# Performance work log

Hardware: AMD Instinct MI355X
Metric: run time of the kernel (lower is better)

The kernel has to match this reference:

```python
import jax, jax.numpy as jnp
import numpy as np
from jax import lax

DIM = 256
HEADS = 8
SR = 4
EPS = 1e-5
SCALE = (DIM // HEADS) ** -0.5


def _dwconv(x, wgt, stride, pad):
    # x: (B,C,H,W), wgt: (C,1,kh,kw) depthwise
    return lax.conv_general_dilated(
        x, wgt, (stride, stride), [(pad, pad), (pad, pad)],
        feature_group_count=x.shape[1],
        dimension_numbers=("NCHW", "OIHW", "NCHW"))


def _bn(x, g, b, m, v):
    # eval-mode batchnorm folded to per-channel scale/shift
    s = g / jnp.sqrt(v + EPS)
    return x * s[:, None, None] + (b - m * s)[:, None, None]


def setup_inputs() -> dict:
    key = jax.random.key(0)
    ks = jax.random.split(key, 16)
    b, h, w = 8, 64, 64
    c = DIM
    n = h * w

    def rn(k, shape, s=0.05):
        return jax.random.normal(k, shape, jnp.float32) * s

    return dict(
        x=jax.random.normal(ks[0], (b, n, c), jnp.float32),
        h=h, w=w,
        Wq=rn(ks[1], (c, c)), bq=rn(ks[2], (c,)),
        Wkv=rn(ks[3], (2 * c, c)), bkv=rn(ks[4], (2 * c,)),
        sr_w1=rn(ks[5], (c, 1, SR + 3, SR + 3), 0.1),
        bn1_gamma=1.0 + rn(ks[6], (c,)), bn1_beta=rn(ks[7], (c,)),
        bn1_mean=rn(ks[8], (c,)), bn1_var=jnp.abs(1.0 + rn(ks[9], (c,))),
        sr_w2=1.0 + rn(ks[10], (c,), 0.2),  # 1x1 depthwise conv == per-channel scale
        bn2_gamma=1.0 + rn(ks[11], (c,)), bn2_beta=rn(ks[12], (c,)),
        bn2_mean=rn(ks[13], (c,)), bn2_var=jnp.abs(1.0 + rn(ks[14], (c,))),
        local_w=rn(ks[15], (c, 1, 3, 3), 0.1),
        local_b=jnp.zeros((c,), jnp.float32),
    )


def reference(x, h, w, Wq, bq, Wkv, bkv, sr_w1, bn1_gamma, bn1_beta, bn1_mean,
              bn1_var, sr_w2, bn2_gamma, bn2_beta, bn2_mean, bn2_var,
              local_w, local_b):
    b, n, c = x.shape
    hd = c // HEADS
    xi = x.transpose(0, 2, 1).reshape(b, c, h, w)  # (b,c,h,w)

    # q projection (1x1 conv == channel matmul)
    q = jnp.einsum("bchw,dc->bdhw", xi, Wq) + bq[None, :, None, None]
    q = q.reshape(b, HEADS, hd, n).transpose(0, 1, 3, 2)  # (b,H,n,hd)

    # spatial reduction: dwconv7 s4 + BN + GELU + dw1x1 + BN
    kv = _dwconv(xi, sr_w1, SR, (SR + 3) // 2)
    kv = _bn(kv, bn1_gamma, bn1_beta, bn1_mean, bn1_var)
    kv = jax.nn.gelu(kv, approximate=False)
    kv = kv * sr_w2[None, :, None, None]
    kv = _bn(kv, bn2_gamma, bn2_beta, bn2_mean, bn2_var)

    # residual local depthwise 3x3 conv
    kv = _dwconv(kv, local_w, 1, 1) + local_b[None, :, None, None] + kv

    # kv projection and split
    kvp = jnp.einsum("bchw,dc->bdhw", kv, Wkv) + bkv[None, :, None, None]
    k_, v_ = jnp.split(kvp, 2, axis=1)
    m = k_.shape[2] * k_.shape[3]
    k_ = k_.reshape(b, HEADS, hd, m)                       # (b,H,hd,m)
    v_ = v_.reshape(b, HEADS, hd, m).transpose(0, 1, 3, 2)  # (b,H,m,hd)

    attn = jax.nn.softmax(jnp.einsum("bhnd,bhdm->bhnm", q, k_) * SCALE, axis=-1)
    out = jnp.einsum("bhnm,bhmd->bhnd", attn, v_)           # (b,H,n,hd)
    out = out.transpose(0, 1, 3, 2).reshape(b, c, n).transpose(0, 2, 1)
    return out
```

## Files before the change

### kernel.cpp

```cpp
#include <hip/hip_runtime.h>
#include <math.h>

typedef __bf16 bf16;
typedef bf16 bf16x4 __attribute__((ext_vector_type(4)));
typedef bf16 bf16x8 __attribute__((ext_vector_type(8)));
typedef float f32x4 __attribute__((ext_vector_type(4)));

static_assert(sizeof(bf16x8) == 16, "bf16x8 must be 16B");

#define QSCALE (0.17677669529663687f * 1.4426950408889634f)

__device__ __forceinline__ f32x4 mfma16(bf16x8 a, bf16x8 b, f32x4 c) {
  return __builtin_amdgcn_mfma_f32_16x16x32_bf16(a, b, c, 0, 0, 0);
}

__global__ __launch_bounds__(256) void k_cvt(
    const float* __restrict__ Wq, const float* __restrict__ Wkv,
    const float* __restrict__ w7, bf16* __restrict__ Wqb,
    bf16* __restrict__ Wkvb, float* __restrict__ w7t) {
  const int tid = threadIdx.x;
  const int blk = blockIdx.x;
  if (blk < 96) {
    const float* src;
    bf16* dst;
    if (blk < 32) {
      const int idx = blk * 256 + tid;
      src = Wq + (size_t)idx * 8;
      dst = Wqb + (size_t)idx * 8;
    } else {
      const int idx = (blk - 32) * 256 + tid;
      src = Wkv + (size_t)idx * 8;
      dst = Wkvb + (size_t)idx * 8;
    }
    const float4 a = ((const float4*)src)[0];
    const float4 b = ((const float4*)src)[1];
    bf16x8 r;
    r[0] = (bf16)a.x; r[1] = (bf16)a.y; r[2] = (bf16)a.z; r[3] = (bf16)a.w;
    r[4] = (bf16)b.x; r[5] = (bf16)b.y; r[6] = (bf16)b.z; r[7] = (bf16)b.w;
    *(bf16x8*)dst = r;
  } else {
    const int c = tid;
    #pragma unroll
    for (int tap = 0; tap < 49; tap++)
      w7t[tap * 256 + c] = w7[c * 49 + tap];
  }
}

__global__ __launch_bounds__(256) void k_sr(
    const float* __restrict__ x, const float* __restrict__ w7t,
    const float* __restrict__ g1, const float* __restrict__ b1,
    const float* __restrict__ m1, const float* __restrict__ v1,
    const float* __restrict__ sw2,
    const float* __restrict__ g2, const float* __restrict__ b2,
    const float* __restrict__ m2, const float* __restrict__ v2,
    bf16* __restrict__ kv1) {
  __shared__ float part[4][256];
  const int tid = threadIdx.x;
  const int team = tid >> 6, g = tid & 63;
  const int c0 = g * 4;
  const int blk = blockIdx.x;
  const int b = blk & 7, m = blk >> 3;
  const int oy = m >> 4, ox = m & 15;

  float4 xv[13], wv[13];
  float msk[13];
  #pragma unroll
  for (int j = 0; j < 13; j++) {
    const int tap = team + j * 4;
    const int ky = tap / 7, kx = tap - ky * 7;
    const int iy = oy * 4 - 3 + ky, ix = ox * 4 - 3 + kx;
    msk[j] = (tap < 49 && iy >= 0 && iy < 64 && ix >= 0 && ix < 64) ? 1.f : 0.f;
    const int iyc = iy < 0 ? 0 : (iy > 63 ? 63 : iy);
    const int ixc = ix < 0 ? 0 : (ix > 63 ? 63 : ix);
    const int tc = tap > 48 ? 48 : tap;
    xv[j] = *(const float4*)(x + ((size_t)b * 4096 + iyc * 64 + ixc) * 256 + c0);
    wv[j] = *(const float4*)(w7t + tc * 256 + c0);
  }
  float a0 = 0.f, a1 = 0.f, a2 = 0.f, a3 = 0.f;
  #pragma unroll
  for (int j = 0; j < 13; j++) {
    a0 += xv[j].x * wv[j].x * msk[j];
    a1 += xv[j].y * wv[j].y * msk[j];
    a2 += xv[j].z * wv[j].z * msk[j];
    a3 += xv[j].w * wv[j].w * msk[j];
  }
  *(f32x4*)&part[team][c0] = (f32x4){a0, a1, a2, a3};
  __syncthreads();
  const int c = tid;
  float y = part[0][c] + part[1][c] + part[2][c] + part[3][c];
  float s = g1[c] / sqrtf(v1[c] + 1e-5f);
  y = y * s + (b1[c] - m1[c] * s);
  y = 0.5f * y * (1.f + erff(y * 0.70710678118654752f));
  y *= sw2[c];
  s = g2[c] / sqrtf(v2[c] + 1e-5f);
  y = y * s + (b2[c] - m2[c] * s);
  kv1[((size_t)b * 256 + m) * 256 + c] = (bf16)y;
}

__global__ __launch_bounds__(256) void k_localkv(
    const bf16* __restrict__ kv1, const float* __restrict__ w3,
    const float* __restrict__ lb, const bf16* __restrict__ Wkvb,
    const float* __restrict__ bkv, bf16* __restrict__ k_a,
    bf16* __restrict__ v_b) {
  __shared__ bf16 halo[3][10][256];
  __shared__ float rows[8][256];
  const int c = threadIdx.x;
  const int mt = blockIdx.x;
  const int b = blockIdx.y;
  const int oy = mt >> 1, o0 = (mt & 1) * 8;

  #pragma unroll
  for (int p = 0; p < 30; p++) {
    const int dy = p / 10, xi = p - dy * 10;
    const int iy = oy - 1 + dy, ix = o0 - 1 + xi;
    const bool ok = (iy >= 0 && iy < 16 && ix >= 0 && ix < 16);
    const int iyc = ok ? iy : 0, ixc = ok ? ix : 0;
    const bf16 v = kv1[((size_t)b * 256 + iyc * 16 + ixc) * 256 + c];
    halo[dy][xi][c] = ok ? v : (bf16)0.f;
  }
  float w3f[9];
  #pragma unroll
  for (int t = 0; t < 9; t++) w3f[t] = w3[c * 9 + t];
  const float lbf = lb[c];
  __syncthreads();

  #pragma unroll
  for (int r = 0; r < 8; r++) {
    float acc = lbf + (float)halo[1][r + 1][c];
    #pragma unroll
    for (int ky = 0; ky < 3; ky++)
      #pragma unroll
      for (int kx = 0; kx < 3; kx++)
        acc += (float)halo[ky][r + kx][c] * w3f[ky * 3 + kx];
    rows[r][c] = acc;
  }
  __syncthreads();

  const int tid = c;
  float acck[8] = {0}, accv[8] = {0};
  for (int oc = 0; oc < 32; oc++) {
    const bf16x8 w0 = *(const bf16x8*)(Wkvb + (size_t)tid * 256 + oc * 8);
    const bf16x8 w1 = *(const bf16x8*)(Wkvb + ((size_t)tid + 256) * 256 + oc * 8);
    float wf0[8], wf1[8];
    #pragma unroll
    for (int j = 0; j < 8; j++) { wf0[j] = (float)w0[j]; wf1[j] = (float)w1[j]; }
    #pragma unroll
    for (int r = 0; r < 8; r++) {
      const float4* rp = (const float4*)&rows[r][oc * 8];
      const float4 ra = rp[0], rb = rp[1];
      const float rv[8] = {ra.x, ra.y, ra.z, ra.w, rb.x, rb.y, rb.z, rb.w};
      #pragma unroll
      for (int j = 0; j < 8; j++) {
        acck[r] += wf0[j] * rv[j];
        accv[r] += wf1[j] * rv[j];
      }
    }
  }
  const float bk = bkv[tid], bv = bkv[tid + 256];
  const int h = tid >> 5, d = tid & 31;
  #pragma unroll
  for (int r = 0; r < 8; r++) {
    const int m = (oy * 16 + o0) + r;
    k_a[(((size_t)b * 8 + h) * 256 + m) * 32 + d] = (bf16)(acck[r] + bk);
    v_b[(((size_t)b * 8 + h) * 32 + d) * 256 + m] = (bf16)(accv[r] + bv);
  }
}

__global__ __launch_bounds__(256) void k_qproj(
    const float* __restrict__ x, const bf16* __restrict__ Wqb,
    const float* __restrict__ bq, bf16* __restrict__ q_ws) {
  __shared__ bf16 xs[32 * 264];
  const int tid = threadIdx.x, wv = tid >> 6, lane = tid & 63;
  const int qd = lane >> 4, l15 = lane & 15;
  const size_t rowbase = (size_t)blockIdx.x * 32;

  #pragma unroll
  for (int it = 0; it < 4; it++) {
    const int idx = it * 256 + tid;
    const int lr = idx >> 5, pos = idx & 31;
    const float* src = x + (rowbase + lr) * 256 + pos * 8;
    const float4 a = ((const float4*)src)[0];
    const float4 b = ((const float4*)src)[1];
    bf16x8 r;
    r[0] = (bf16)a.x; r[1] = (bf16)a.y; r[2] = (bf16)a.z; r[3] = (bf16)a.w;
    r[4] = (bf16)b.x; r[5] = (bf16)b.y; r[6] = (bf16)b.z; r[7] = (bf16)b.w;
    *(bf16x8*)(xs + lr * 264 + pos * 8) = r;
  }
  __syncthreads();

  f32x4 acc0[4], acc1[4];
  #pragma unroll
  for (int dt = 0; dt < 4; dt++) {
    acc0[dt] = (f32x4){0.f, 0.f, 0.f, 0.f};
    acc1[dt] = (f32x4){0.f, 0.f, 0.f, 0.f};
  }
  #pragma unroll 2
  for (int kc = 0; kc < 8; kc++) {
    const bf16x8 a0 = *(const bf16x8*)(xs + l15 * 264 + kc * 32 + qd * 8);
    const bf16x8 a1 = *(const bf16x8*)(xs + (16 + l15) * 264 + kc * 32 + qd * 8);
    #pragma unroll
    for (int dt = 0; dt < 4; dt++) {
      const int d = wv * 64 + dt * 16 + l15;
      const bf16x8 bb = *(const bf16x8*)(Wqb + (size_t)d * 256 + kc * 32 + qd * 8);
      acc0[dt] = mfma16(a0, bb, acc0[dt]);
      acc1[dt] = mfma16(a1, bb, acc1[dt]);
    }
  }
  #pragma unroll
  for (int dt = 0; dt < 4; dt++) {
    const int d = wv * 64 + dt * 16 + l15;
    const float bias = bq[d];
    const int h = d >> 5, dl = d & 31;
    #pragma unroll
    for (int r = 0; r < 4; r++) {
      const size_t row0 = rowbase + qd * 4 + r;
      const size_t row1 = rowbase + 16 + qd * 4 + r;
      q_ws[(((row0 >> 12) * 8 + h) * 4096 + (row0 & 4095)) * 32 + dl] =
          (bf16)((acc0[dt][r] + bias) * QSCALE);
      q_ws[(((row1 >> 12) * 8 + h) * 4096 + (row1 & 4095)) * 32 + dl] =
          (bf16)((acc1[dt][r] + bias) * QSCALE);
    }
  }
}

__global__ __launch_bounds__(256) void k_attn(
    const bf16* __restrict__ q_ws, const bf16* __restrict__ k_a,
    const bf16* __restrict__ v_b, float* __restrict__ out) {
  const int tid = threadIdx.x;
  const int wv = tid >> 6, lane = tid & 63;
  const int qd = lane >> 4, l15 = lane & 15;
  const int b = blockIdx.z, h = blockIdx.y;
  const int bh = b * 8 + h;
  const int n_base = blockIdx.x * 256 + wv * 64;

  const bf16* qb = q_ws + ((size_t)bh * 4096 + n_base) * 32;
  bf16x8 qf[4];
  #pragma unroll
  for (int qi = 0; qi < 4; qi++)
    qf[qi] = *(const bf16x8*)(qb + (size_t)(qi * 16 + l15) * 32 + qd * 8);

  const bf16* kb = k_a + (size_t)bh * 256 * 32;
  const bf16* vb = v_b + (size_t)bh * 32 * 256;

  f32x4 acc[4][2];
  float lr[4] = {0.f, 0.f, 0.f, 0.f};
  #pragma unroll
  for (int qi = 0; qi < 4; qi++) {
    acc[qi][0] = (f32x4){0.f, 0.f, 0.f, 0.f};
    acc[qi][1] = (f32x4){0.f, 0.f, 0.f, 0.f};
  }
  const int kperm = 8 * (l15 >> 2) + (l15 & 3);

  bf16x8 ka0 = *(const bf16x8*)(kb + (size_t)kperm * 32 + qd * 8);
  bf16x8 ka1 = *(const bf16x8*)(kb + (size_t)(kperm + 4) * 32 + qd * 8);
  bf16x8 va0 = *(const bf16x8*)(vb + (size_t)l15 * 256 + qd * 8);
  bf16x8 va1 = *(const bf16x8*)(vb + (size_t)(16 + l15) * 256 + qd * 8);

  for (int ch = 0; ch < 8; ch++) {
    const int cn = (ch < 7 ? ch + 1 : 7) * 32;
    const bf16x8 nk0 = *(const bf16x8*)(kb + (size_t)(cn + kperm) * 32 + qd * 8);
    const bf16x8 nk1 = *(const bf16x8*)(kb + (size_t)(cn + kperm + 4) * 32 + qd * 8);
    const bf16x8 nv0 = *(const bf16x8*)(vb + (size_t)l15 * 256 + cn + qd * 8);
    const bf16x8 nv1 = *(const bf16x8*)(vb + (size_t)(16 + l15) * 256 + cn + qd * 8);
    const f32x4 z = (f32x4){0.f, 0.f, 0.f, 0.f};
    #pragma unroll
    for (int qi = 0; qi < 4; qi++) {
      f32x4 s0 = mfma16(ka0, qf[qi], z);
      f32x4 s1 = mfma16(ka1, qf[qi], z);
      float p[8], ls = 0.f;
      #pragma unroll
      for (int j = 0; j < 4; j++) {
        p[j] = __builtin_amdgcn_exp2f(fminf(s0[j], 80.f));
        p[4 + j] = __builtin_amdgcn_exp2f(fminf(s1[j], 80.f));
      }
      #pragma unroll
      for (int j = 0; j < 8; j++) ls += p[j];
      lr[qi] += ls;
      bf16x8 pb;
      #pragma unroll
      for (int j = 0; j < 8; j++) pb[j] = (bf16)p[j];
      acc[qi][0] = mfma16(va0, pb, acc[qi][0]);
      acc[qi][1] = mfma16(va1, pb, acc[qi][1]);
    }
    ka0 = nk0; ka1 = nk1; va0 = nv0; va1 = nv1;
  }
  #pragma unroll
  for (int qi = 0; qi < 4; qi++) {
    float l = lr[qi];
    l += __shfl_xor(l, 16, 64);
    l += __shfl_xor(l, 32, 64);
    const float inv = 1.f / l;
    const int nn = n_base + qi * 16 + l15;
    float* ob = out + (size_t)(b * 4096 + nn) * 256 + h * 32;
    #pragma unroll
    for (int t = 0; t < 2; t++) {
      *(float4*)(ob + t * 16 + qd * 4) =
          (float4){acc[qi][t][0] * inv, acc[qi][t][1] * inv,
                   acc[qi][t][2] * inv, acc[qi][t][3] * inv};
    }
  }
}

extern "C" void kernel_launch(void* const* d_in, const int* in_sizes, int n_in,
                              void* d_out, int out_size, void* d_ws, size_t ws_size,
                              hipStream_t stream) {
  const float* x      = (const float*)d_in[0];
  const float* Wq     = (const float*)d_in[3];
  const float* bq     = (const float*)d_in[4];
  const float* Wkv    = (const float*)d_in[5];
  const float* bkv    = (const float*)d_in[6];
  const float* sr_w1  = (const float*)d_in[7];
  const float* bn1_g  = (const float*)d_in[8];
  const float* bn1_b  = (const float*)d_in[9];
  const float* bn1_m  = (const float*)d_in[10];
  const float* bn1_v  = (const float*)d_in[11];
  const float* sw2    = (const float*)d_in[12];
  const float* bn2_g  = (const float*)d_in[13];
  const float* bn2_b  = (const float*)d_in[14];
  const float* bn2_m  = (const float*)d_in[15];
  const float* bn2_v  = (const float*)d_in[16];
  const float* lw     = (const float*)d_in[17];
  const float* lb     = (const float*)d_in[18];

  const int B = in_sizes[0] / (4096 * 256);

  bf16* Wqb  = (bf16*)d_ws;
  bf16* Wkvb = Wqb + 65536;
  float* w7t = (float*)(Wkvb + 131072);
  bf16* kv1  = (bf16*)(w7t + 12544);
  bf16* k_a  = kv1 + (size_t)B * 256 * 256;
  bf16* v_b  = k_a + (size_t)B * 8 * 256 * 32;
  bf16* q_ws = v_b + (size_t)B * 8 * 32 * 256;

  k_cvt<<<dim3(97), 256, 0, stream>>>(Wq, Wkv, sr_w1, Wqb, Wkvb, w7t);
  k_sr<<<dim3(256 * B), 256, 0, stream>>>(x, w7t, bn1_g, bn1_b, bn1_m, bn1_v,
                                          sw2, bn2_g, bn2_b, bn2_m, bn2_v, kv1);
  k_localkv<<<dim3(32, B), 256, 0, stream>>>(kv1, lw, lb, Wkvb, bkv, k_a, v_b);
  k_qproj<<<dim3(B * 128), 256, 0, stream>>>(x, Wqb, bq, q_ws);
  k_attn<<<dim3(16, 8, B), 256, 0, stream>>>(q_ws, k_a, v_b, (float*)d_out);
}
```

Baseline: 186.7 us.

## Fuse q projection into attention and merge weight conversion with spatial reduction

The q projection is now computed inside the attention kernel for each (batch, head, 256-row tile). x is staged through shared memory as bf16, and the scaled q values are placed in LDS instead of a global workspace. This removes the q workspace write and read and one launch, but each x tile is now re-read once per head. The weight-conversion kernel is merged with the spatial-reduction kernel, and the 7x7 weight transpose pass is dropped in favour of strided reads of the original weights. This saves another launch and a small workspace.

```diff
diff --git a/kernel.cpp b/kernel.cpp
--- a/kernel.cpp
+++ b/kernel.cpp
@@ -14,21 +14,30 @@
   return __builtin_amdgcn_mfma_f32_16x16x32_bf16(a, b, c, 0, 0, 0);
 }
 
-__global__ __launch_bounds__(256) void k_cvt(
+__global__ __launch_bounds__(256) void k_pre(
+    const float* __restrict__ x, const float* __restrict__ w7,
+    const float* __restrict__ g1, const float* __restrict__ b1,
+    const float* __restrict__ m1, const float* __restrict__ v1,
+    const float* __restrict__ sw2,
+    const float* __restrict__ g2, const float* __restrict__ b2,
+    const float* __restrict__ m2, const float* __restrict__ v2,
     const float* __restrict__ Wq, const float* __restrict__ Wkv,
-    const float* __restrict__ w7, bf16* __restrict__ Wqb,
-    bf16* __restrict__ Wkvb, float* __restrict__ w7t) {
+    bf16* __restrict__ Wqb, bf16* __restrict__ Wkvb,
+    bf16* __restrict__ kv1, int nsr) {
+  __shared__ float part[4][256];
   const int tid = threadIdx.x;
   const int blk = blockIdx.x;
-  if (blk < 96) {
+
+  if (blk >= nsr) {
+    const int wb = blk - nsr;
     const float* src;
     bf16* dst;
-    if (blk < 32) {
-      const int idx = blk * 256 + tid;
+    if (wb < 32) {
+      const int idx = wb * 256 + tid;
       src = Wq + (size_t)idx * 8;
       dst = Wqb + (size_t)idx * 8;
     } else {
-      const int idx = (blk - 32) * 256 + tid;
+      const int idx = (wb - 32) * 256 + tid;
       src = Wkv + (size_t)idx * 8;
       dst = Wkvb + (size_t)idx * 8;
     }
@@ -38,32 +47,15 @@
     r[0] = (bf16)a.x; r[1] = (bf16)a.y; r[2] = (bf16)a.z; r[3] = (bf16)a.w;
     r[4] = (bf16)b.x; r[5] = (bf16)b.y; r[6] = (bf16)b.z; r[7] = (bf16)b.w;
     *(bf16x8*)dst = r;
-  } else {
-    const int c = tid;
-    #pragma unroll
-    for (int tap = 0; tap < 49; tap++)
-      w7t[tap * 256 + c] = w7[c * 49 + tap];
-  }
-}
-
-__global__ __launch_bounds__(256) void k_sr(
-    const float* __restrict__ x, const float* __restrict__ w7t,
-    const float* __restrict__ g1, const float* __restrict__ b1,
-    const float* __restrict__ m1, const float* __restrict__ v1,
-    const float* __restrict__ sw2,
-    const float* __restrict__ g2, const float* __restrict__ b2,
-    const float* __restrict__ m2, const float* __restrict__ v2,
-    bf16* __restrict__ kv1) {
-  __shared__ float part[4][256];
-  const int tid = threadIdx.x;
+    return;
+  }
   const int team = tid >> 6, g = tid & 63;
   const int c0 = g * 4;
-  const int blk = blockIdx.x;
   const int b = blk & 7, m = blk >> 3;
   const int oy = m >> 4, ox = m & 15;
 
-  float4 xv[13], wv[13];
-  float msk[13];
+  float4 xv[13];
+  float wj[13][4], msk[13];
   #pragma unroll
   for (int j = 0; j < 13; j++) {
     const int tap = team + j * 4;
@@ -74,15 +66,16 @@
     const int ixc = ix < 0 ? 0 : (ix > 63 ? 63 : ix);
     const int tc = tap > 48 ? 48 : tap;
     xv[j] = *(const float4*)(x + ((size_t)b * 4096 + iyc * 64 + ixc) * 256 + c0);
-    wv[j] = *(const float4*)(w7t + tc * 256 + c0);
+    #pragma unroll
+    for (int i = 0; i < 4; i++) wj[j][i] = w7[(c0 + i) * 49 + tc];
   }
   float a0 = 0.f, a1 = 0.f, a2 = 0.f, a3 = 0.f;
   #pragma unroll
   for (int j = 0; j < 13; j++) {
-    a0 += xv[j].x * wv[j].x * msk[j];
-    a1 += xv[j].y * wv[j].y * msk[j];
-    a2 += xv[j].z * wv[j].z * msk[j];
-    a3 += xv[j].w * wv[j].w * msk[j];
+    a0 += xv[j].x * wj[j][0] * msk[j];
+    a1 += xv[j].y * wj[j][1] * msk[j];
+    a2 += xv[j].z * wj[j][2] * msk[j];
+    a3 += xv[j].w * wj[j][3] * msk[j];
   }
   *(f32x4*)&part[team][c0] = (f32x4){a0, a1, a2, a3};
   __syncthreads();
@@ -166,78 +159,66 @@
   }
 }
 
-__global__ __launch_bounds__(256) void k_qproj(
+__global__ __launch_bounds__(256) void k_qattn(
     const float* __restrict__ x, const bf16* __restrict__ Wqb,
-    const float* __restrict__ bq, bf16* __restrict__ q_ws) {
-  __shared__ bf16 xs[32 * 264];
-  const int tid = threadIdx.x, wv = tid >> 6, lane = tid & 63;
-  const int qd = lane >> 4, l15 = lane & 15;
-  const size_t rowbase = (size_t)blockIdx.x * 32;
-
-  #pragma unroll
-  for (int it = 0; it < 4; it++) {
-    const int idx = it * 256 + tid;
-    const int lr = idx >> 5, pos = idx & 31;
-    const float* src = x + (rowbase + lr) * 256 + pos * 8;
-    const float4 a = ((const float4*)src)[0];
-    const float4 b = ((const float4*)src)[1];
-    bf16x8 r;
-    r[0] = (bf16)a.x; r[1] = (bf16)a.y; r[2] = (bf16)a.z; r[3] = (bf16)a.w;
-    r[4] = (bf16)b.x; r[5] = (bf16)b.y; r[6] = (bf16)b.z; r[7] = (bf16)b.w;
-    *(bf16x8*)(xs + lr * 264 + pos * 8) = r;
-  }
-  __syncthreads();
-
-  f32x4 acc0[4], acc1[4];
-  #pragma unroll
-  for (int dt = 0; dt < 4; dt++) {
-    acc0[dt] = (f32x4){0.f, 0.f, 0.f, 0.f};
-    acc1[dt] = (f32x4){0.f, 0.f, 0.f, 0.f};
-  }
-  #pragma unroll 2
-  for (int kc = 0; kc < 8; kc++) {
-    const bf16x8 a0 = *(const bf16x8*)(xs + l15 * 264 + kc * 32 + qd * 8);
-    const bf16x8 a1 = *(const bf16x8*)(xs + (16 + l15) * 264 + kc * 32 + qd * 8);
-    #pragma unroll
-    for (int dt = 0; dt < 4; dt++) {
-      const int d = wv * 64 + dt * 16 + l15;
-      const bf16x8 bb = *(const bf16x8*)(Wqb + (size_t)d * 256 + kc * 32 + qd * 8);
-      acc0[dt] = mfma16(a0, bb, acc0[dt]);
-      acc1[dt] = mfma16(a1, bb, acc1[dt]);
-    }
-  }
-  #pragma unroll
-  for (int dt = 0; dt < 4; dt++) {
-    const int d = wv * 64 + dt * 16 + l15;
-    const float bias = bq[d];
-    const int h = d >> 5, dl = d & 31;
-    #pragma unroll
-    for (int r = 0; r < 4; r++) {
-      const size_t row0 = rowbase + qd * 4 + r;
-      const size_t row1 = rowbase + 16 + qd * 4 + r;
-      q_ws[(((row0 >> 12) * 8 + h) * 4096 + (row0 & 4095)) * 32 + dl] =
-          (bf16)((acc0[dt][r] + bias) * QSCALE);
-      q_ws[(((row1 >> 12) * 8 + h) * 4096 + (row1 & 4095)) * 32 + dl] =
-          (bf16)((acc1[dt][r] + bias) * QSCALE);
-    }
-  }
-}
-
-__global__ __launch_bounds__(256) void k_attn(
-    const bf16* __restrict__ q_ws, const bf16* __restrict__ k_a,
+    const float* __restrict__ bq, const bf16* __restrict__ k_a,
     const bf16* __restrict__ v_b, float* __restrict__ out) {
+  __shared__ bf16 xs[256 * 40];
   const int tid = threadIdx.x;
   const int wv = tid >> 6, lane = tid & 63;
   const int qd = lane >> 4, l15 = lane & 15;
-  const int b = blockIdx.z, h = blockIdx.y;
+  const int nt = blockIdx.x, h = blockIdx.y, b = blockIdx.z;
   const int bh = b * 8 + h;
-  const int n_base = blockIdx.x * 256 + wv * 64;
-
-  const bf16* qb = q_ws + ((size_t)bh * 4096 + n_base) * 32;
+  const size_t brow0 = (size_t)b * 4096 + nt * 256;
+
+  f32x4 dq0[4], dq1[4];
+  #pragma unroll
+  for (int qi = 0; qi < 4; qi++) {
+    dq0[qi] = (f32x4){0.f, 0.f, 0.f, 0.f};
+    dq1[qi] = (f32x4){0.f, 0.f, 0.f, 0.f};
+  }
+  for (int kc = 0; kc < 8; kc++) {
+    __syncthreads();
+    #pragma unroll
+    for (int j = 0; j < 8; j++) {
+      const int e = j * 1024 + tid * 4;
+      const int r = e >> 5, c = e & 31;
+      const float4 v = *(const float4*)(x + (brow0 + r) * 256 + kc * 32 + c);
+      bf16x4 bv;
+      bv[0] = (bf16)v.x; bv[1] = (bf16)v.y; bv[2] = (bf16)v.z; bv[3] = (bf16)v.w;
+      *(bf16x4*)(xs + r * 40 + c) = bv;
+    }
+    __syncthreads();
+    const bf16x8 a0 = *(const bf16x8*)(Wqb + (size_t)(h * 32 + l15) * 256 + kc * 32 + qd * 8);
+    const bf16x8 a1 = *(const bf16x8*)(Wqb + (size_t)(h * 32 + 16 + l15) * 256 + kc * 32 + qd * 8);
+    #pragma unroll
+    for (int qi = 0; qi < 4; qi++) {
+      const bf16x8 bb = *(const bf16x8*)(xs + (wv * 64 + qi * 16 + l15) * 40 + qd * 8);
+      dq0[qi] = mfma16(a0, bb, dq0[qi]);
+      dq1[qi] = mfma16(a1, bb, dq1[qi]);
+    }
+  }
+  const float4 bq0 = *(const float4*)(bq + h * 32 + qd * 4);
+  const float4 bq1 = *(const float4*)(bq + h * 32 + 16 + qd * 4);
+  bf16* ql = xs + (size_t)wv * 64 * 40;
+  #pragma unroll
+  for (int qi = 0; qi < 4; qi++) {
+    bf16x4 q0, q1;
+    q0[0] = (bf16)((dq0[qi][0] + bq0.x) * QSCALE);
+    q0[1] = (bf16)((dq0[qi][1] + bq0.y) * QSCALE);
+    q0[2] = (bf16)((dq0[qi][2] + bq0.z) * QSCALE);
+    q0[3] = (bf16)((dq0[qi][3] + bq0.w) * QSCALE);
+    q1[0] = (bf16)((dq1[qi][0] + bq1.x) * QSCALE);
+    q1[1] = (bf16)((dq1[qi][1] + bq1.y) * QSCALE);
+    q1[2] = (bf16)((dq1[qi][2] + bq1.z) * QSCALE);
+    q1[3] = (bf16)((dq1[qi][3] + bq1.w) * QSCALE);
+    *(bf16x4*)(ql + (qi * 16 + l15) * 40 + qd * 4) = q0;
+    *(bf16x4*)(ql + (qi * 16 + l15) * 40 + 16 + qd * 4) = q1;
+  }
   bf16x8 qf[4];
   #pragma unroll
   for (int qi = 0; qi < 4; qi++)
-    qf[qi] = *(const bf16x8*)(qb + (size_t)(qi * 16 + l15) * 32 + qd * 8);
+    qf[qi] = *(const bf16x8*)(ql + (qi * 16 + l15) * 40 + qd * 8);
 
   const bf16* kb = k_a + (size_t)bh * 256 * 32;
   const bf16* vb = v_b + (size_t)bh * 32 * 256;
@@ -290,7 +271,7 @@
     l += __shfl_xor(l, 16, 64);
     l += __shfl_xor(l, 32, 64);
     const float inv = 1.f / l;
-    const int nn = n_base + qi * 16 + l15;
+    const int nn = nt * 256 + wv * 64 + qi * 16 + l15;
     float* ob = out + (size_t)(b * 4096 + nn) * 256 + h * 32;
     #pragma unroll
     for (int t = 0; t < 2; t++) {
@@ -326,16 +307,16 @@
 
   bf16* Wqb  = (bf16*)d_ws;
   bf16* Wkvb = Wqb + 65536;
-  float* w7t = (float*)(Wkvb + 131072);
-  bf16* kv1  = (bf16*)(w7t + 12544);
+  bf16* kv1  = Wkvb + 131072;
   bf16* k_a  = kv1 + (size_t)B * 256 * 256;
   bf16* v_b  = k_a + (size_t)B * 8 * 256 * 32;
-  bf16* q_ws = v_b + (size_t)B * 8 * 32 * 256;
-
-  k_cvt<<<dim3(97), 256, 0, stream>>>(Wq, Wkv, sr_w1, Wqb, Wkvb, w7t);
-  k_sr<<<dim3(256 * B), 256, 0, stream>>>(x, w7t, bn1_g, bn1_b, bn1_m, bn1_v,
-                                          sw2, bn2_g, bn2_b, bn2_m, bn2_v, kv1);
+
+  const int nsr = 256 * B;
+
+  k_pre<<<dim3(nsr + 96), 256, 0, stream>>>(
+      x, sr_w1, bn1_g, bn1_b, bn1_m, bn1_v, sw2, bn2_g, bn2_b, bn2_m, bn2_v,
+      Wq, Wkv, Wqb, Wkvb, kv1, nsr);
   k_localkv<<<dim3(32, B), 256, 0, stream>>>(kv1, lw, lb, Wkvb, bkv, k_a, v_b);
-  k_qproj<<<dim3(B * 128), 256, 0, stream>>>(x, Wqb, bq, q_ws);
-  k_attn<<<dim3(16, 8, B), 256, 0, stream>>>(q_ws, k_a, v_b, (float*)d_out);
-}
+  k_qattn<<<dim3(16, 8, B), 256, 0, stream>>>(x, Wqb, bq, k_a, v_b,
+                                              (float*)d_out);
+}
```

New measurement: 232.0 us. 1.24x slower.

## Merge weight conversion with SR conv and fuse localkv with qproj launch

Applied to the files above, without the earlier changes.

The weight-convert kernel and the spatial-reduction conv kernel are combined into one launch, and the local-conv/kv-projection and q-projection kernels share a second launch selected by block index. The 7x7 weight transpose pass is dropped: each team now handles a contiguous run of taps and reads the weights straight from the original layout. Going from five launches to three is meant to cut launch overhead and tail gaps and to let the independent q projection overlap the small kv work. In exchange, the per-thread weight reads are strided and uncoalesced, and the combined kernels have to reserve the larger shared-memory footprint.

```diff
diff --git a/kernel.cpp b/kernel.cpp
--- a/kernel.cpp
+++ b/kernel.cpp
@@ -14,21 +14,30 @@
   return __builtin_amdgcn_mfma_f32_16x16x32_bf16(a, b, c, 0, 0, 0);
 }
 
-__global__ __launch_bounds__(256) void k_cvt(
+__global__ __launch_bounds__(256) void k_pre(
+    const float* __restrict__ x, const float* __restrict__ w7,
+    const float* __restrict__ g1, const float* __restrict__ b1,
+    const float* __restrict__ m1, const float* __restrict__ v1,
+    const float* __restrict__ sw2,
+    const float* __restrict__ g2, const float* __restrict__ b2,
+    const float* __restrict__ m2, const float* __restrict__ v2,
     const float* __restrict__ Wq, const float* __restrict__ Wkv,
-    const float* __restrict__ w7, bf16* __restrict__ Wqb,
-    bf16* __restrict__ Wkvb, float* __restrict__ w7t) {
+    bf16* __restrict__ Wqb, bf16* __restrict__ Wkvb,
+    bf16* __restrict__ kv1, int nsr) {
+  __shared__ float part[4][256];
   const int tid = threadIdx.x;
   const int blk = blockIdx.x;
-  if (blk < 96) {
+
+  if (blk >= nsr) {
+    const int wb = blk - nsr;
     const float* src;
     bf16* dst;
-    if (blk < 32) {
-      const int idx = blk * 256 + tid;
+    if (wb < 32) {
+      const int idx = wb * 256 + tid;
       src = Wq + (size_t)idx * 8;
       dst = Wqb + (size_t)idx * 8;
     } else {
-      const int idx = (blk - 32) * 256 + tid;
+      const int idx = (wb - 32) * 256 + tid;
       src = Wkv + (size_t)idx * 8;
       dst = Wkvb + (size_t)idx * 8;
     }
@@ -38,51 +47,42 @@
     r[0] = (bf16)a.x; r[1] = (bf16)a.y; r[2] = (bf16)a.z; r[3] = (bf16)a.w;
     r[4] = (bf16)b.x; r[5] = (bf16)b.y; r[6] = (bf16)b.z; r[7] = (bf16)b.w;
     *(bf16x8*)dst = r;
-  } else {
-    const int c = tid;
-    #pragma unroll
-    for (int tap = 0; tap < 49; tap++)
-      w7t[tap * 256 + c] = w7[c * 49 + tap];
-  }
-}
-
-__global__ __launch_bounds__(256) void k_sr(
-    const float* __restrict__ x, const float* __restrict__ w7t,
-    const float* __restrict__ g1, const float* __restrict__ b1,
-    const float* __restrict__ m1, const float* __restrict__ v1,
-    const float* __restrict__ sw2,
-    const float* __restrict__ g2, const float* __restrict__ b2,
-    const float* __restrict__ m2, const float* __restrict__ v2,
-    bf16* __restrict__ kv1) {
-  __shared__ float part[4][256];
-  const int tid = threadIdx.x;
+    return;
+  }
   const int team = tid >> 6, g = tid & 63;
   const int c0 = g * 4;
-  const int blk = blockIdx.x;
+  const int base = (team == 0) ? 0 : (1 + team * 12);
+  const int cnt  = (team == 0) ? 13 : 12;
   const int b = blk & 7, m = blk >> 3;
   const int oy = m >> 4, ox = m & 15;
 
-  float4 xv[13], wv[13];
+  float w[4][13];
+  #pragma unroll
+  for (int i = 0; i < 4; i++) {
+    const float* wp = w7 + (size_t)(c0 + i) * 49 + base;
+    #pragma unroll
+    for (int j = 0; j < 12; j++) w[i][j] = wp[j];
+    w[i][12] = wp[cnt == 13 ? 12 : 11];
+  }
+  float4 xv[13];
   float msk[13];
   #pragma unroll
   for (int j = 0; j < 13; j++) {
-    const int tap = team + j * 4;
+    const int tap = base + (j < cnt ? j : 0);
     const int ky = tap / 7, kx = tap - ky * 7;
     const int iy = oy * 4 - 3 + ky, ix = ox * 4 - 3 + kx;
-    msk[j] = (tap < 49 && iy >= 0 && iy < 64 && ix >= 0 && ix < 64) ? 1.f : 0.f;
+    msk[j] = (j < cnt && iy >= 0 && iy < 64 && ix >= 0 && ix < 64) ? 1.f : 0.f;
     const int iyc = iy < 0 ? 0 : (iy > 63 ? 63 : iy);
     const int ixc = ix < 0 ? 0 : (ix > 63 ? 63 : ix);
-    const int tc = tap > 48 ? 48 : tap;
     xv[j] = *(const float4*)(x + ((size_t)b * 4096 + iyc * 64 + ixc) * 256 + c0);
-    wv[j] = *(const float4*)(w7t + tc * 256 + c0);
   }
   float a0 = 0.f, a1 = 0.f, a2 = 0.f, a3 = 0.f;
   #pragma unroll
   for (int j = 0; j < 13; j++) {
-    a0 += xv[j].x * wv[j].x * msk[j];
-    a1 += xv[j].y * wv[j].y * msk[j];
-    a2 += xv[j].z * wv[j].z * msk[j];
-    a3 += xv[j].w * wv[j].w * msk[j];
+    a0 += xv[j].x * w[0][j] * msk[j];
+    a1 += xv[j].y * w[1][j] * msk[j];
+    a2 += xv[j].z * w[2][j] * msk[j];
+    a3 += xv[j].w * w[3][j] * msk[j];
   }
   *(f32x4*)&part[team][c0] = (f32x4){a0, a1, a2, a3};
   __syncthreads();
@@ -97,16 +97,15 @@
   kv1[((size_t)b * 256 + m) * 256 + c] = (bf16)y;
 }
 
-__global__ __launch_bounds__(256) void k_localkv(
+__device__ __forceinline__ void localkv_body(
+    char* smem, int mt, int b,
     const bf16* __restrict__ kv1, const float* __restrict__ w3,
     const float* __restrict__ lb, const bf16* __restrict__ Wkvb,
     const float* __restrict__ bkv, bf16* __restrict__ k_a,
     bf16* __restrict__ v_b) {
-  __shared__ bf16 halo[3][10][256];
-  __shared__ float rows[8][256];
+  bf16 (*halo)[10][256] = (bf16(*)[10][256])smem;
+  float (*rows)[256] = (float(*)[256])(smem + 15360);
   const int c = threadIdx.x;
-  const int mt = blockIdx.x;
-  const int b = blockIdx.y;
   const int oy = mt >> 1, o0 = (mt & 1) * 8;
 
   #pragma unroll
@@ -166,13 +165,14 @@
   }
 }
 
-__global__ __launch_bounds__(256) void k_qproj(
+__device__ __forceinline__ void qproj_body(
+    char* smem, int qblk,
     const float* __restrict__ x, const bf16* __restrict__ Wqb,
     const float* __restrict__ bq, bf16* __restrict__ q_ws) {
-  __shared__ bf16 xs[32 * 264];
+  bf16* xs = (bf16*)smem;
   const int tid = threadIdx.x, wv = tid >> 6, lane = tid & 63;
   const int qd = lane >> 4, l15 = lane & 15;
-  const size_t rowbase = (size_t)blockIdx.x * 32;
+  const size_t rowbase = (size_t)qblk * 32;
 
   #pragma unroll
   for (int it = 0; it < 4; it++) {
@@ -221,6 +221,21 @@
           (bf16)((acc1[dt][r] + bias) * QSCALE);
     }
   }
+}
+
+__global__ __launch_bounds__(256) void k_mid(
+    const bf16* __restrict__ kv1, const float* __restrict__ w3,
+    const float* __restrict__ lb, const bf16* __restrict__ Wkvb,
+    const float* __restrict__ bkv, bf16* __restrict__ k_a,
+    bf16* __restrict__ v_b,
+    const float* __restrict__ x, const bf16* __restrict__ Wqb,
+    const float* __restrict__ bq, bf16* __restrict__ q_ws) {
+  __shared__ char smem[23552];
+  const int blk = blockIdx.x;
+  if (blk < 256)
+    localkv_body(smem, blk & 31, blk >> 5, kv1, w3, lb, Wkvb, bkv, k_a, v_b);
+  else
+    qproj_body(smem, blk - 256, x, Wqb, bq, q_ws);
 }
 
 __global__ __launch_bounds__(256) void k_attn(
@@ -326,16 +341,17 @@
 
   bf16* Wqb  = (bf16*)d_ws;
   bf16* Wkvb = Wqb + 65536;
-  float* w7t = (float*)(Wkvb + 131072);
-  bf16* kv1  = (bf16*)(w7t + 12544);
+  bf16* kv1  = Wkvb + 131072;
   bf16* k_a  = kv1 + (size_t)B * 256 * 256;
   bf16* v_b  = k_a + (size_t)B * 8 * 256 * 32;
   bf16* q_ws = v_b + (size_t)B * 8 * 32 * 256;
 
-  k_cvt<<<dim3(97), 256, 0, stream>>>(Wq, Wkv, sr_w1, Wqb, Wkvb, w7t);
-  k_sr<<<dim3(256 * B), 256, 0, stream>>>(x, w7t, bn1_g, bn1_b, bn1_m, bn1_v,
-                                          sw2, bn2_g, bn2_b, bn2_m, bn2_v, kv1);
-  k_localkv<<<dim3(32, B), 256, 0, stream>>>(kv1, lw, lb, Wkvb, bkv, k_a, v_b);
-  k_qproj<<<dim3(B * 128), 256, 0, stream>>>(x, Wqb, bq, q_ws);
+  const int nsr = 256 * B;
+
+  k_pre<<<dim3(nsr + 96), 256, 0, stream>>>(
+      x, sr_w1, bn1_g, bn1_b, bn1_m, bn1_v, sw2, bn2_g, bn2_b, bn2_m, bn2_v,
+      Wq, Wkv, Wqb, Wkvb, kv1, nsr);
+  k_mid<<<dim3(256 + B * 128), 256, 0, stream>>>(
+      kv1, lw, lb, Wkvb, bkv, k_a, v_b, x, Wqb, bq, q_ws);
   k_attn<<<dim3(16, 8, B), 256, 0, stream>>>(q_ws, k_a, v_b, (float*)d_out);
 }
```

Result: slower. 204.1 us (+9.3%).
